# Kernel tuning notes

Measured on AMD Instinct MI355X. Metric: run time of the kernel, lower is better.

The kernel has to match this reference:

```python
import jax, jax.numpy as jnp
import numpy as np

K = 20
EPS = 1e-5
NEG_SLOPE = 0.2


def _graph_feature(x, k):
    # x: [B, N, C] -> edge features [B, N, k, 2C]
    xx = jnp.sum(x * x, axis=-1)                       # [B, N]
    inner = jnp.einsum('bnc,bmc->bnm', x, x)           # [B, N, N]
    neg_dist = 2.0 * inner - xx[:, :, None] - xx[:, None, :]
    idx = jax.lax.top_k(neg_dist, k)[1]                # [B, N, k] nearest neighbors
    nbr = jax.vmap(lambda f, i: f[i])(x, idx)          # [B, N, k, C]
    center = jnp.broadcast_to(x[:, :, None, :], nbr.shape)
    return jnp.concatenate([nbr - center, center], axis=-1)


def _bn(y, gamma, beta, axes):
    mu = y.mean(axes, keepdims=True)
    var = y.var(axes, keepdims=True)
    return (y - mu) * jax.lax.rsqrt(var + EPS) * gamma + beta


def _lrelu(y):
    return jnp.where(y > 0, y, NEG_SLOPE * y)


def _edge_block(feat, w, gamma, beta):
    # feat: [B, N, k, Cin], w: [Cout, Cin] (1x1 conv)
    y = jnp.einsum('bnkc,oc->bnko', feat, w)
    y = _lrelu(_bn(y, gamma, beta, (0, 1, 2)))
    return y.max(axis=2)                               # max over k -> [B, N, Cout]


def setup_inputs() -> dict:
    key = jax.random.key(0)
    ks = jax.random.split(key, 8)
    B, N = 16, 2048
    num_features = 128
    x = jax.random.normal(ks[0], (B, N, 3), dtype=jnp.float32)
    s = 0.05
    w1 = jax.random.normal(ks[1], (64, 6), dtype=jnp.float32) * s
    w2 = jax.random.normal(ks[2], (64, 128), dtype=jnp.float32) * s
    w3 = jax.random.normal(ks[3], (128, 128), dtype=jnp.float32) * s
    w4 = jax.random.normal(ks[4], (256, 256), dtype=jnp.float32) * s
    w5 = jax.random.normal(ks[5], (512, 512), dtype=jnp.float32) * s
    we = jax.random.normal(ks[6], (num_features, 512), dtype=jnp.float32) * s
    def gb(c):
        return jnp.ones((c,), jnp.float32), jnp.zeros((c,), jnp.float32)
    g1, b1 = gb(64); g2, b2 = gb(64); g3, b3 = gb(128); g4, b4 = gb(256); g5, b5 = gb(512)
    return dict(x=x, w1=w1, g1=g1, b1=b1, w2=w2, g2=g2, b2=b2, w3=w3, g3=g3, b3=b3,
                w4=w4, g4=g4, b4=b4, w5=w5, g5=g5, b5=b5, we=we)


def reference(x, w1, g1, b1, w2, g2, b2, w3, g3, b3, w4, g4, b4, w5, g5, b5, we):
    # x: [B, N, 3]
    x1 = _edge_block(_graph_feature(x, K), w1, g1, b1)    # [B, N, 64]
    x2 = _edge_block(_graph_feature(x1, K), w2, g2, b2)   # [B, N, 64]
    x3 = _edge_block(_graph_feature(x2, K), w3, g3, b3)   # [B, N, 128]
    x4 = _edge_block(_graph_feature(x3, K), w4, g4, b4)   # [B, N, 256]
    cat = jnp.concatenate([x1, x2, x3, x4], axis=-1)      # [B, N, 512]
    y = jnp.einsum('bnc,oc->bno', cat, w5)                # conv5 (1x1 conv1d)
    y = _lrelu(_bn(y, g5, b5, (0, 1)))
    y = y.max(axis=1)                                     # global max pool -> [B, 512]
    return y @ we.T                                       # embedding -> [B, num_features]
```

## Files before the change

kernel.cpp:

```cpp
#include <hip/hip_runtime.h>
#include <hip/hip_bf16.h>
#include <cstdint>

#define B_ 16
#define N_ 2048
#define KNN_K 20
#define EPS_ 1e-5f
#define SLOPE_ 0.2f
#define IMS 4.8828125e-4f

typedef __attribute__((ext_vector_type(4))) float f32x4;
typedef __attribute__((ext_vector_type(8))) short bf16x8;
typedef __attribute__((ext_vector_type(8))) _Float16 f16x8;

static __device__ __forceinline__ float lrelu(float v){ return v > 0.f ? v : SLOPE_*v; }

static __device__ __forceinline__ unsigned encf(float f){
  unsigned b = __float_as_uint(f);
  return (b & 0x80000000u) ? ~b : (b | 0x80000000u);
}
static __device__ __forceinline__ float decf(unsigned u){
  unsigned b = (u & 0x80000000u) ? (u ^ 0x80000000u) : ~u;
  return __uint_as_float(b);
}
static __device__ __forceinline__ short bfbits(float v){
  __hip_bfloat16 h = __float2bfloat16(v);
  return *reinterpret_cast<short*>(&h);
}
static __device__ __forceinline__ short h16(float v){
  _Float16 h = (_Float16)v;
  return *reinterpret_cast<short*>(&h);
}
static __device__ __forceinline__ float h2f(short s){
  _Float16 h = *reinterpret_cast<_Float16*>(&s);
  return (float)h;
}

template<int C, int CP>
__global__ __launch_bounds__(256) void convert_kernel(const float* __restrict__ f, int lda,
                                                      short* __restrict__ fbf, size_t plane,
                                                      float* __restrict__ xx){
  int wid  = (blockIdx.x * 256 + threadIdx.x) >> 6;
  int lane = threadIdx.x & 63;
  if (wid >= B_*N_) return;
  const float* p = f + (size_t)wid*lda;
  float s = 0.f;
  for (int c = lane; c < CP; c += 64){
    float v = (c < C) ? p[c] : 0.f;
    short h = h16(v);
    short m = h16((v - h2f(h)) * 2048.f);
    size_t o = (size_t)wid*CP + c;
    fbf[o] = h;
    fbf[plane + o] = m;
    s += v*v;
  }
  #pragma unroll
  for (int off=32; off; off>>=1) s += __shfl_down(s, off);
  if (lane==0) xx[wid] = s;
}

template<int CP>
__global__ __launch_bounds__(256) void knn_mfma(const short* __restrict__ fbf, size_t plane,
                                                const float* __restrict__ xx,
                                                float* __restrict__ pval, int* __restrict__ pidx){
  constexpr int SP = CP + 8;
  constexpr int CH = CP/8;
  constexpr int KC = CP/32;
  constexpr int PFH = CP/32;
  constexpr int FMBS = 2*64*SP;
  constexpr bool ALIAS = (FMBS*2 >= 64*65*4);
  constexpr unsigned LDSB = ALIAS ? (unsigned)(FMBS*2) : (unsigned)(FMBS*2 + 64*65*4);
  __shared__ __align__(16) char ldsbuf[LDSB];
  short* fmb = (short*)ldsbuf;
  float* dtile = ALIAS ? (float*)ldsbuf : (float*)(ldsbuf + FMBS*2);
  __shared__ float xm_s[64];

  int b   = blockIdx.x >> 6;
  int rem = blockIdx.x & 63;
  int n0  = (rem >> 1) << 6;
  int mh  = rem & 1;
  int mbase = mh << 10;
  int tid = threadIdx.x;
  int w    = tid >> 6;
  int lane = tid & 63;
  int fr = lane & 15, hi = lane >> 4;
  int r_loc = lane >> 2, csub = lane & 3;
  int gb = lane & 60;
  int myrow = w*16 + r_loc;
  size_t browoff = (size_t)b * N_;

  f16x8 aH[KC], aM[KC];
  {
    size_t arow = (browoff + n0 + w*16 + fr) * (size_t)CP;
    #pragma unroll
    for (int kc=0; kc<KC; ++kc){
      aH[kc] = *(const f16x8*)&fbf[arow + kc*32 + hi*8];
      aM[kc] = *(const f16x8*)&fbf[plane + arow + kc*32 + hi*8];
    }
  }

  float sv[5]; int si[5];
  #pragma unroll
  for (int j=0;j<5;++j){ sv[j] = -1e30f; si[j] = 0x7FFFFFFF; }

  int ldso[PFH];
  const short* gH[PFH];
  const short* gM[PFH];
  #pragma unroll
  for (int j=0;j<PFH;++j){
    int i = tid + j*256;
    int r = i/CH, cq = i - r*CH;
    ldso[j] = r*SP + cq*8;
    size_t g0 = (browoff + mbase + r)*(size_t)CP + cq*8;
    gH[j] = fbf + g0;
    gM[j] = fbf + plane + g0;
  }
  const float* xmp = xx + browoff + mbase + (tid & 63);
  float xmreg = 0.f;

  f16x8 pf[PFH];
  auto PFLOAD = [&](){
    #pragma unroll
    for (int j=0;j<PFH;++j) pf[j] = *(const f16x8*)gH[j];
    if (tid < 64) xmreg = *xmp;
  };
  auto WRITEPF = [&](){
    #pragma unroll
    for (int j=0;j<PFH;++j) *(f16x8*)&fmb[ldso[j]] = pf[j];
    #pragma unroll
    for (int j=0;j<PFH;++j){
      f16x8 v = *(const f16x8*)gM[j];
      *(f16x8*)&fmb[64*SP + ldso[j]] = v;
      gM[j] += 64*CP;
    }
    #pragma unroll
    for (int j=0;j<PFH;++j) gH[j] += 64*CP;
    if (tid < 64) xm_s[tid] = xmreg;
    xmp += 64;
  };

  PFLOAD();
  WRITEPF();
  __syncthreads();

  for (int mt = 0; mt < 16; ++mt){
    int m0 = mbase + (mt << 6);
    if (mt + 1 < 16) PFLOAD();

    f32x4 accH[4], accM[4];
    #pragma unroll
    for (int ct=0; ct<4; ++ct){ accH[ct] = (f32x4){0.f,0.f,0.f,0.f}; accM[ct] = accH[ct]; }
    const short* BH = fmb;
    const short* BM = fmb + 64*SP;
    #pragma unroll
    for (int kc = 0; kc < KC; ++kc){
      #pragma unroll
      for (int ct=0; ct<4; ++ct){
        int boff = (ct*16 + fr)*SP + kc*32 + hi*8;
        f16x8 bh = *(const f16x8*)&BH[boff];
        f16x8 bm = *(const f16x8*)&BM[boff];
        accH[ct] = __builtin_amdgcn_mfma_f32_16x16x32_f16(aH[kc], bh, accH[ct], 0,0,0);
        accM[ct] = __builtin_amdgcn_mfma_f32_16x16x32_f16(aM[kc], bh, accM[ct], 0,0,0);
        accM[ct] = __builtin_amdgcn_mfma_f32_16x16x32_f16(aH[kc], bm, accM[ct], 0,0,0);
      }
    }
    __syncthreads();

    #pragma unroll
    for (int reg=0; reg<4; ++reg){
      int nl = w*16 + hi*4 + reg;
      #pragma unroll
      for (int ct=0; ct<4; ++ct)
        dtile[nl*65 + ct*16 + fr] = 2.f*(accH[ct][reg] + IMS*accM[ct][reg]) - xm_s[ct*16 + fr];
    }

    int base = myrow*65 + csub*16;
    float thr = __shfl(sv[4], lane | 3);
    unsigned qm = 0u;
    #pragma unroll
    for (int jj=0; jj<16; ++jj){
      float v = dtile[base + jj];
      qm |= (v > thr) ? (1u << jj) : 0u;
    }
    unsigned long long bal = __ballot(qm != 0u);
    while (bal){
      unsigned nib = (unsigned)((bal >> gb) & 0xFull);
      int leader = nib ? (gb + (int)__builtin_ctz(nib)) : 64;
      int bbit = (int)__builtin_ctz(qm | 0x10000u);
      float mv = dtile[base + (bbit & 15)];
      int mid = m0 + (csub << 4) + bbit;
      float cv = __shfl(mv, leader);
      int   cid = __shfl(mid, leader);
      qm = (lane == leader) ? (qm & (qm - 1u)) : qm;
      int cnt = 0;
      #pragma unroll
      for (int j=0;j<5;++j) cnt += (sv[j] >= cv) ? 1 : 0;
      cnt += __shfl_xor(cnt, 1);
      cnt += __shfl_xor(cnt, 2);
      int pos = nib ? cnt : 20;
      float pv = __shfl_up(sv[4], 1);
      int   pi = __shfl_up(si[4], 1);
      #pragma unroll
      for (int j=0;j<5;++j){
        int g = csub*5 + j;
        float ns = (g < pos) ? sv[j] : ((g == pos) ? cv : pv);
        int   ni = (g < pos) ? si[j] : ((g == pos) ? cid : pi);
        pv = sv[j]; pi = si[j];
        sv[j] = ns; si[j] = ni;
      }
      bal = __ballot(qm != 0u);
    }

    if (mt + 1 < 16){
      if constexpr (ALIAS){
        __syncthreads();
        WRITEPF();
        __syncthreads();
      } else {
        WRITEPF();
        __syncthreads();
      }
    }
  }

  size_t orow = browoff + n0 + myrow;
  float* pvo = pval + (orow*2 + mh)*KNN_K + csub*5;
  int*   pio = pidx + (orow*2 + mh)*KNN_K + csub*5;
  #pragma unroll
  for (int j=0;j<5;++j){ pvo[j] = sv[j]; pio[j] = si[j]; }
}

__global__ __launch_bounds__(256) void knn_merge(const float* __restrict__ pval,
                                                 const int* __restrict__ pidx,
                                                 int* __restrict__ idxout){
  int r = blockIdx.x*256 + threadIdx.x;
  if (r >= B_*N_) return;
  const float* va = pval + (size_t)r*2*KNN_K;
  const float* vb = va + KNN_K;
  const int*   ia = pidx + (size_t)r*2*KNN_K;
  const int*   ib = ia + KNN_K;
  int i=0, j=0;
  #pragma unroll
  for (int t=0;t<KNN_K;++t){
    float a = va[i], bq = vb[j];
    bool ta = (a >= bq);
    idxout[(size_t)r*KNN_K + t] = ta ? ia[i] : ib[j];
    i += ta ? 1 : 0; j += ta ? 0 : 1;
  }
}

template<int CP>
__global__ __launch_bounds__(256) void gemm_pq(const short* __restrict__ fbf, size_t plane,
                                               const float* __restrict__ Wsrc, int wstride, int Cin,
                                               float* __restrict__ Out, int O){
  constexpr int BK = (CP < 64) ? CP : 64;
  constexpr int SP = BK + 8;
  __shared__ short Ah[128*SP];
  __shared__ short Am[128*SP];
  __shared__ short Wh[64*SP];
  __shared__ short Wm[64*SP];
  int obl = O >> 6;
  int bo = ((int)blockIdx.x % obl) << 6;
  int bm = ((int)blockIdx.x / obl) << 7;
  int tid = threadIdx.x;
  int w = tid >> 6, lane = tid & 63;
  int fr = lane & 15, hi = lane >> 4;
  f32x4 accH[2][4], accM[2][4];
  #pragma unroll
  for (int g=0; g<2; ++g)
    #pragma unroll
    for (int ct=0; ct<4; ++ct){ accH[g][ct] = (f32x4){0.f,0.f,0.f,0.f}; accM[g][ct] = accH[g][ct]; }

  for (int k0=0; k0<CP; k0+=BK){
    __syncthreads();
    for (int i=tid; i < 128*(BK/8); i += 256){
      int r = i/(BK/8), cq = i%(BK/8);
      size_t src = ((size_t)bm + r)*CP + k0 + cq*8;
      *(f16x8*)&Ah[r*SP + cq*8] = *(const f16x8*)&fbf[src];
      *(f16x8*)&Am[r*SP + cq*8] = *(const f16x8*)&fbf[plane + src];
    }
    for (int i=tid; i < 64*(BK/8); i += 256){
      int r = i/(BK/8), cq = i%(BK/8);
      f16x8 vh, vm;
      #pragma unroll
      for (int e=0;e<8;++e){
        int c = k0 + cq*8 + e;
        float v = (c < Cin) ? Wsrc[(size_t)(bo + r)*wstride + c] : 0.f;
        _Float16 h = (_Float16)v;
        vh[e] = h;
        vm[e] = (_Float16)((v - (float)h) * 2048.f);
      }
      *(f16x8*)&Wh[r*SP + cq*8] = vh;
      *(f16x8*)&Wm[r*SP + cq*8] = vm;
    }
    __syncthreads();
    #pragma unroll
    for (int kc=0; kc<BK/32; ++kc){
      f16x8 a0h = *(const f16x8*)&Ah[(w*32 +      fr)*SP + kc*32 + hi*8];
      f16x8 a0m = *(const f16x8*)&Am[(w*32 +      fr)*SP + kc*32 + hi*8];
      f16x8 a1h = *(const f16x8*)&Ah[(w*32 + 16 + fr)*SP + kc*32 + hi*8];
      f16x8 a1m = *(const f16x8*)&Am[(w*32 + 16 + fr)*SP + kc*32 + hi*8];
      #pragma unroll
      for (int ct=0; ct<4; ++ct){
        f16x8 bh = *(const f16x8*)&Wh[(ct*16 + fr)*SP + kc*32 + hi*8];
        f16x8 bm = *(const f16x8*)&Wm[(ct*16 + fr)*SP + kc*32 + hi*8];
        accH[0][ct] = __builtin_amdgcn_mfma_f32_16x16x32_f16(a0h, bh, accH[0][ct], 0,0,0);
        accM[0][ct] = __builtin_amdgcn_mfma_f32_16x16x32_f16(a0m, bh, accM[0][ct], 0,0,0);
        accM[0][ct] = __builtin_amdgcn_mfma_f32_16x16x32_f16(a0h, bm, accM[0][ct], 0,0,0);
        accH[1][ct] = __builtin_amdgcn_mfma_f32_16x16x32_f16(a1h, bh, accH[1][ct], 0,0,0);
        accM[1][ct] = __builtin_amdgcn_mfma_f32_16x16x32_f16(a1m, bh, accM[1][ct], 0,0,0);
        accM[1][ct] = __builtin_amdgcn_mfma_f32_16x16x32_f16(a1h, bm, accM[1][ct], 0,0,0);
      }
    }
  }
  #pragma unroll
  for (int g=0; g<2; ++g)
    #pragma unroll
    for (int ct=0; ct<4; ++ct)
      #pragma unroll
      for (int reg=0; reg<4; ++reg){
        int row = bm + w*32 + g*16 + hi*4 + reg;
        Out[(size_t)row*O + bo + ct*16 + fr] = accH[g][ct][reg] + IMS*accM[g][ct][reg];
      }
}

__global__ __launch_bounds__(256) void gemm_bf16(const float* __restrict__ A,
                                                 const float* __restrict__ Wt,
                                                 float* __restrict__ C){
  __shared__ short As[128*72];
  __shared__ short Bs[64*72];
  int bm = (int)(blockIdx.x >> 3) << 7;
  int bo = (int)(blockIdx.x & 7) << 6;
  int tid = threadIdx.x;
  int w = tid >> 6, lane = tid & 63;
  int fr = lane & 15, hi = lane >> 4;
  f32x4 acc[2][4];
  #pragma unroll
  for (int g=0; g<2; ++g)
    #pragma unroll
    for (int ct=0; ct<4; ++ct) acc[g][ct] = (f32x4){0.f,0.f,0.f,0.f};

  for (int k0=0; k0<512; k0+=64){
    __syncthreads();
    #pragma unroll 2
    for (int i = tid; i < 1024; i += 256){
      int r = i >> 3, cq = i & 7;
      const float* src = &A[(size_t)(bm + r)*512 + k0 + cq*8];
      bf16x8 v;
      #pragma unroll
      for (int e=0;e<8;++e) v[e] = bfbits(src[e]);
      *(bf16x8*)&As[r*72 + cq*8] = v;
    }
    #pragma unroll 2
    for (int i = tid; i < 512; i += 256){
      int r = i >> 3, cq = i & 7;
      const float* src = &Wt[(size_t)(bo + r)*512 + k0 + cq*8];
      bf16x8 v;
      #pragma unroll
      for (int e=0;e<8;++e) v[e] = bfbits(src[e]);
      *(bf16x8*)&Bs[r*72 + cq*8] = v;
    }
    __syncthreads();
    #pragma unroll
    for (int kc=0; kc<2; ++kc){
      bf16x8 a0 = *(const bf16x8*)&As[(w*32 +      fr)*72 + kc*32 + hi*8];
      bf16x8 a1 = *(const bf16x8*)&As[(w*32 + 16 + fr)*72 + kc*32 + hi*8];
      #pragma unroll
      for (int ct=0; ct<4; ++ct){
        bf16x8 bb = *(const bf16x8*)&Bs[(ct*16 + fr)*72 + kc*32 + hi*8];
        acc[0][ct] = __builtin_amdgcn_mfma_f32_16x16x32_bf16(a0, bb, acc[0][ct], 0,0,0);
        acc[1][ct] = __builtin_amdgcn_mfma_f32_16x16x32_bf16(a1, bb, acc[1][ct], 0,0,0);
      }
    }
  }
  #pragma unroll
  for (int g=0; g<2; ++g)
    #pragma unroll
    for (int ct=0; ct<4; ++ct)
      #pragma unroll
      for (int reg=0; reg<4; ++reg){
        int row = bm + w*32 + g*16 + hi*4 + reg;
        C[(size_t)row*512 + bo + ct*16 + fr] = acc[g][ct][reg];
      }
}

__global__ void wq_kernel(const float* __restrict__ w, float* __restrict__ wq, int Cin, int O){
  int i = blockIdx.x*blockDim.x + threadIdx.x;
  if (i >= O*Cin) return;
  int o = i / Cin, c = i - o*Cin;
  wq[i] = w[(size_t)o*2*Cin + Cin + c] - w[(size_t)o*2*Cin + c];
}

__global__ void zero_f_kernel(float* p, int n){
  int i = blockIdx.x*blockDim.x + threadIdx.x;
  if (i < n) p[i] = 0.f;
}
__global__ void zero_u_kernel(unsigned* p, int n){
  int i = blockIdx.x*blockDim.x + threadIdx.x;
  if (i < n) p[i] = 0u;
}

__global__ __launch_bounds__(256) void edge_agg(const float* __restrict__ P, const float* __restrict__ Q,
      const int* __restrict__ idx, const float* __restrict__ gamma,
      float* __restrict__ S, float* __restrict__ sums, float* __restrict__ sumsq, int O){
  const int ROWS = 64;
  int rpi = 256 / O;
  int iters = ROWS / rpi;
  int row0 = blockIdx.x * ROWS;
  int tid = threadIdx.x;
  int o  = tid % O;
  int rl = tid / O;
  int b  = row0 / N_;
  __shared__ int sidx[4][KNN_K];
  __shared__ float s1[256], s2[256];
  float g = gamma[o];
  float csum=0.f, csumsq=0.f;
  for (int it=0; it<iters; ++it){
    __syncthreads();
    if (tid < KNN_K*rpi) sidx[tid/KNN_K][tid%KNN_K] = idx[(size_t)(row0 + it*rpi)*KNN_K + tid];
    __syncthreads();
    int row = row0 + it*rpi + rl;
    float q = Q[(size_t)row*O + o];
    float mx=-1e30f, mn=1e30f, s=0.f, ss=0.f;
    #pragma unroll
    for (int k=0;k<KNN_K;++k){
      int m = sidx[rl][k];
      float p = P[((size_t)b*N_ + m)*O + o];
      mx = fmaxf(mx,p); mn = fminf(mn,p);
      float y = p + q; s += y; ss += y*y;
    }
    csum += s; csumsq += ss;
    S[(size_t)row*O + o] = (g >= 0.f ? mx : mn) + q;
  }
  s1[tid]=0.f; s2[tid]=0.f;
  __syncthreads();
  atomicAdd(&s1[o], csum); atomicAdd(&s2[o], csumsq);
  __syncthreads();
  if (tid < O){ atomicAdd(&sums[tid], s1[tid]); atomicAdd(&sumsq[tid], s2[tid]); }
}

__global__ void bn_finalize(const float* __restrict__ sums, const float* __restrict__ sumsq,
                            const float* __restrict__ gamma, const float* __restrict__ beta,
                            float invM, float* __restrict__ scale, float* __restrict__ shift, int O){
  int o = blockIdx.x*blockDim.x + threadIdx.x;
  if (o >= O) return;
  float mu = sums[o]*invM;
  float var = sumsq[o]*invM - mu*mu;
  float rs = rsqrtf(var + EPS_);
  float sc = gamma[o]*rs;
  scale[o] = sc; shift[o] = beta[o] - mu*sc;
}

__global__ void apply_write(const float* __restrict__ S, const float* __restrict__ scale,
                            const float* __restrict__ shift, float* __restrict__ cat, int off, int O){
  int i = blockIdx.x*blockDim.x + threadIdx.x;
  if (i >= B_*N_*O) return;
  int row = i / O, o = i - row*O;
  float v = S[i]*scale[o] + shift[o];
  cat[(size_t)row*512 + off + o] = lrelu(v);
}

__global__ __launch_bounds__(256) void conv5_stats(const float* __restrict__ Y, const float* __restrict__ g5,
      float* __restrict__ sums, float* __restrict__ sumsq, unsigned* __restrict__ maxenc){
  int bb = blockIdx.x / 16;
  int n0 = (blockIdx.x % 16) * 128;
  int tid = threadIdx.x;
  float s0=0.f, s1=0.f, q0=0.f, q1=0.f, m0=-1e30f, m1=-1e30f;
  float ga = g5[tid], gb = g5[tid+256];
  for (int n=0;n<128;++n){
    size_t base = ((size_t)bb*N_ + n0 + n)*512;
    float ya = Y[base + tid];
    float yb = Y[base + tid + 256];
    s0 += ya; q0 += ya*ya;
    s1 += yb; q1 += yb*yb;
    m0 = fmaxf(m0, ga>=0.f ? ya : -ya);
    m1 = fmaxf(m1, gb>=0.f ? yb : -yb);
  }
  atomicAdd(&sums[tid],      s0); atomicAdd(&sumsq[tid],      q0);
  atomicAdd(&sums[tid+256],  s1); atomicAdd(&sumsq[tid+256],  q1);
  atomicMax(&maxenc[bb*512 + tid],       encf(m0));
  atomicMax(&maxenc[bb*512 + tid + 256], encf(m1));
}

__global__ void pool_kernel(const unsigned* __restrict__ maxenc, const float* __restrict__ scale,
                            const float* __restrict__ shift, const float* __restrict__ g5,
                            float* __restrict__ pooled){
  int i = blockIdx.x*blockDim.x + threadIdx.x;
  if (i >= B_*512) return;
  int o = i & 511;
  float t = decf(maxenc[i]);
  float y = g5[o] >= 0.f ? t : -t;
  pooled[i] = lrelu(y*scale[o] + shift[o]);
}

__global__ void final_mm(const float* __restrict__ pooled, const float* __restrict__ we,
                         float* __restrict__ out){
  int i = blockIdx.x*blockDim.x + threadIdx.x;
  if (i >= B_*128) return;
  int b = i >> 7, j = i & 127;
  const float4* pp = (const float4*)(pooled + (size_t)b*512);
  const float4* wp = (const float4*)(we + (size_t)j*512);
  float s = 0.f;
  for (int c=0;c<128;++c){
    float4 a = pp[c], w = wp[c];
    s += a.x*w.x + a.y*w.y + a.z*w.z + a.w*w.w;
  }
  out[i] = s;
}

struct Ws {
  float* cat; float* P; float* Q; float* S; int* idx; float* xx;
  float* sums; float* sumsq; float* scale; float* shift;
  float* wq; unsigned* maxenc; float* pooled; short* fbf;
  float* pval; int* pidx;
};

template<int C, int CP>
static void run_layer(const Ws& W, const float* f, int lda, int O,
                      const float* w, const float* g, const float* bt,
                      int off_out, hipStream_t stream){
  const int M = B_*N_;
  size_t plane = (size_t)M*CP;
  convert_kernel<C, CP><<<M/4, 256, 0, stream>>>(f, lda, W.fbf, plane, W.xx);
  knn_mfma<CP><<<B_*(N_/64)*2, 256, 0, stream>>>(W.fbf, plane, W.xx, W.pval, W.pidx);
  knn_merge<<<(M+255)/256, 256, 0, stream>>>(W.pval, W.pidx, W.idx);
  int nwq = O*C;
  wq_kernel<<<(nwq+255)/256, 256, 0, stream>>>(w, W.wq, C, O);
  int grid = (M/128)*(O/64);
  gemm_pq<CP><<<grid, 256, 0, stream>>>(W.fbf, plane, w,    2*C, C, W.P, O);
  gemm_pq<CP><<<grid, 256, 0, stream>>>(W.fbf, plane, W.wq, C,   C, W.Q, O);
  zero_f_kernel<<<4, 256, 0, stream>>>(W.sums, 1024);
  edge_agg<<<M/64, 256, 0, stream>>>(W.P, W.Q, W.idx, g, W.S, W.sums, W.sumsq, O);
  bn_finalize<<<(O+255)/256, 256, 0, stream>>>(W.sums, W.sumsq, g, bt,
                                               1.f/((float)M*KNN_K), W.scale, W.shift, O);
  apply_write<<<(M*O+255)/256, 256, 0, stream>>>(W.S, W.scale, W.shift, W.cat, off_out, O);
}

extern "C" void kernel_launch(void* const* d_in, const int* in_sizes, int n_in,
                              void* d_out, int out_size, void* d_ws, size_t ws_size,
                              hipStream_t stream) {
  const float* x  = (const float*)d_in[0];
  const float* w1 = (const float*)d_in[1];
  const float* g1 = (const float*)d_in[2];
  const float* b1 = (const float*)d_in[3];
  const float* w2 = (const float*)d_in[4];
  const float* g2 = (const float*)d_in[5];
  const float* b2 = (const float*)d_in[6];
  const float* w3 = (const float*)d_in[7];
  const float* g3 = (const float*)d_in[8];
  const float* b3 = (const float*)d_in[9];
  const float* w4 = (const float*)d_in[10];
  const float* g4 = (const float*)d_in[11];
  const float* b4 = (const float*)d_in[12];
  const float* w5 = (const float*)d_in[13];
  const float* g5 = (const float*)d_in[14];
  const float* b5 = (const float*)d_in[15];
  const float* we = (const float*)d_in[16];

  char* ws = (char*)d_ws;
  Ws W;
  size_t off = 0;
  W.cat   = (float*)(ws + off); off += (size_t)16*2048*512*4;
  W.P     = (float*)(ws + off); off += (size_t)16*2048*256*4;
  W.Q     = (float*)(ws + off); off += (size_t)16*2048*256*4;
  W.S     = (float*)(ws + off); off += (size_t)16*2048*256*4;
  W.idx   = (int*)  (ws + off); off += (size_t)16*2048*20*4;
  W.xx    = (float*)(ws + off); off += (size_t)16*2048*4;
  W.sums  = (float*)(ws + off); off += 512*4;
  W.sumsq = (float*)(ws + off); off += 512*4;
  W.scale = (float*)(ws + off); off += 512*4;
  W.shift = (float*)(ws + off); off += 512*4;
  W.wq    = (float*)(ws + off); off += (size_t)256*128*4;
  W.maxenc= (unsigned*)(ws + off); off += (size_t)16*512*4;
  W.pooled= (float*)(ws + off); off += (size_t)16*512*4;
  W.fbf   = (short*)W.S;
  W.pval  = W.Q;
  W.pidx  = (int*)(W.Q + (size_t)2*16*2048*KNN_K);

  const int M = B_*N_;

  run_layer<3,   32>(W, x,           3,   64,  w1, g1, b1, 0,   stream);
  run_layer<64,  64>(W, W.cat,       512, 64,  w2, g2, b2, 64,  stream);
  run_layer<64,  64>(W, W.cat + 64,  512, 128, w3, g3, b3, 128, stream);
  run_layer<128,128>(W, W.cat + 128, 512, 256, w4, g4, b4, 256, stream);

  float* y5 = W.P;
  gemm_bf16<<<(M/128)*8, 256, 0, stream>>>(W.cat, w5, y5);
  zero_f_kernel<<<4, 256, 0, stream>>>(W.sums, 1024);
  zero_u_kernel<<<32, 256, 0, stream>>>(W.maxenc, 16*512);
  conv5_stats<<<B_*16, 256, 0, stream>>>(y5, g5, W.sums, W.sumsq, W.maxenc);
  bn_finalize<<<2, 256, 0, stream>>>(W.sums, W.sumsq, g5, b5, 1.f/(float)M, W.scale, W.shift, 512);
  pool_kernel<<<(16*512+255)/256, 256, 0, stream>>>(W.maxenc, W.scale, W.shift, g5, W.pooled);
  final_mm<<<(16*128+255)/256, 256, 0, stream>>>(W.pooled, we, (float*)d_out);
}
```

Baseline: 1.215 ms.

## Separate LDS buffers, prefetch both halves early, and rewrite top-k insertion as register max-selection

Gives the distance tile its own LDS region instead of aliasing the feature buffer, which removes one barrier per tile, and moves the low-part (M) global loads into the prefetch phase so both halves are issued before the MFMA loop. The threshold-ballot insertion loop is replaced by per-lane register candidates: each iteration picks the max over a row's four lanes, inserts it, and prunes candidates against the updated threshold. This adds register pressure and LDS usage, which may lower occupancy. The insertion loop may also run more iterations than before.

```diff
diff --git a/kernel.cpp b/kernel.cpp
--- a/kernel.cpp
+++ b/kernel.cpp
@@ -67,12 +67,8 @@
   constexpr int CH = CP/8;
   constexpr int KC = CP/32;
   constexpr int PFH = CP/32;
-  constexpr int FMBS = 2*64*SP;
-  constexpr bool ALIAS = (FMBS*2 >= 64*65*4);
-  constexpr unsigned LDSB = ALIAS ? (unsigned)(FMBS*2) : (unsigned)(FMBS*2 + 64*65*4);
-  __shared__ __align__(16) char ldsbuf[LDSB];
-  short* fmb = (short*)ldsbuf;
-  float* dtile = ALIAS ? (float*)ldsbuf : (float*)(ldsbuf + FMBS*2);
+  __shared__ __align__(16) short fmb[2*64*SP];
+  __shared__ float dtile[64*65];
   __shared__ float xm_s[64];
 
   int b   = blockIdx.x >> 6;
@@ -85,7 +81,6 @@
   int lane = tid & 63;
   int fr = lane & 15, hi = lane >> 4;
   int r_loc = lane >> 2, csub = lane & 3;
-  int gb = lane & 60;
   int myrow = w*16 + r_loc;
   size_t browoff = (size_t)b * N_;
 
@@ -105,36 +100,32 @@
 
   int ldso[PFH];
   const short* gH[PFH];
-  const short* gM[PFH];
   #pragma unroll
   for (int j=0;j<PFH;++j){
     int i = tid + j*256;
     int r = i/CH, cq = i - r*CH;
     ldso[j] = r*SP + cq*8;
-    size_t g0 = (browoff + mbase + r)*(size_t)CP + cq*8;
-    gH[j] = fbf + g0;
-    gM[j] = fbf + plane + g0;
+    gH[j] = fbf + (browoff + mbase + r)*(size_t)CP + cq*8;
   }
   const float* xmp = xx + browoff + mbase + (tid & 63);
   float xmreg = 0.f;
 
-  f16x8 pf[PFH];
+  f16x8 pf[PFH], pm[PFH];
   auto PFLOAD = [&](){
     #pragma unroll
-    for (int j=0;j<PFH;++j) pf[j] = *(const f16x8*)gH[j];
+    for (int j=0;j<PFH;++j){
+      pf[j] = *(const f16x8*)gH[j];
+      pm[j] = *(const f16x8*)(gH[j] + plane);
+    }
     if (tid < 64) xmreg = *xmp;
   };
   auto WRITEPF = [&](){
     #pragma unroll
-    for (int j=0;j<PFH;++j) *(f16x8*)&fmb[ldso[j]] = pf[j];
-    #pragma unroll
     for (int j=0;j<PFH;++j){
-      f16x8 v = *(const f16x8*)gM[j];
-      *(f16x8*)&fmb[64*SP + ldso[j]] = v;
-      gM[j] += 64*CP;
-    }
-    #pragma unroll
-    for (int j=0;j<PFH;++j) gH[j] += 64*CP;
+      *(f16x8*)&fmb[ldso[j]] = pf[j];
+      *(f16x8*)&fmb[64*SP + ldso[j]] = pm[j];
+      gH[j] += 64*CP;
+    }
     if (tid < 64) xm_s[tid] = xmreg;
     xmp += 64;
   };
@@ -164,8 +155,6 @@
         accM[ct] = __builtin_amdgcn_mfma_f32_16x16x32_f16(aH[kc], bm, accM[ct], 0,0,0);
       }
     }
-    __syncthreads();
-
     #pragma unroll
     for (int reg=0; reg<4; ++reg){
       int nl = w*16 + hi*4 + reg;
@@ -173,53 +162,57 @@
       for (int ct=0; ct<4; ++ct)
         dtile[nl*65 + ct*16 + fr] = 2.f*(accH[ct][reg] + IMS*accM[ct][reg]) - xm_s[ct*16 + fr];
     }
+    if (mt + 1 < 16) __syncthreads();
 
     int base = myrow*65 + csub*16;
-    float thr = __shfl(sv[4], lane | 3);
-    unsigned qm = 0u;
-    #pragma unroll
-    for (int jj=0; jj<16; ++jj){
-      float v = dtile[base + jj];
-      qm |= (v > thr) ? (1u << jj) : 0u;
-    }
-    unsigned long long bal = __ballot(qm != 0u);
-    while (bal){
-      unsigned nib = (unsigned)((bal >> gb) & 0xFull);
-      int leader = nib ? (gb + (int)__builtin_ctz(nib)) : 64;
-      int bbit = (int)__builtin_ctz(qm | 0x10000u);
-      float mv = dtile[base + (bbit & 15)];
-      int mid = m0 + (csub << 4) + bbit;
-      float cv = __shfl(mv, leader);
-      int   cid = __shfl(mid, leader);
-      qm = (lane == leader) ? (qm & (qm - 1u)) : qm;
+    float c[16];
+    #pragma unroll
+    for (int jj=0;jj<16;++jj) c[jj] = dtile[base + jj];
+    float t0 = fminf(sv[4], __shfl_xor(sv[4],1));
+    float thr = fminf(t0, __shfl_xor(t0,2));
+    #pragma unroll
+    for (int jj=0;jj<16;++jj) c[jj] = (c[jj] > thr) ? c[jj] : -3e38f;
+
+    while (true){
+      float lv = c[0]; int lj = 0;
+      #pragma unroll
+      for (int jj=1;jj<16;++jj){ bool bt = c[jj] > lv; lv = bt ? c[jj] : lv; lj = bt ? jj : lj; }
+      int lid = m0 + (csub<<4) + lj;
+      float rv = lv; int rid = lid;
+      { float ov = __shfl_xor(rv,1); int oid = __shfl_xor(rid,1);
+        bool tk = (ov > rv) || (ov == rv && oid < rid); rv = tk?ov:rv; rid = tk?oid:rid; }
+      { float ov = __shfl_xor(rv,2); int oid = __shfl_xor(rid,2);
+        bool tk = (ov > rv) || (ov == rv && oid < rid); rv = tk?ov:rv; rid = tk?oid:rid; }
+      if (!__ballot(rv > -2.9e38f)) break;
       int cnt = 0;
       #pragma unroll
-      for (int j=0;j<5;++j) cnt += (sv[j] >= cv) ? 1 : 0;
-      cnt += __shfl_xor(cnt, 1);
-      cnt += __shfl_xor(cnt, 2);
-      int pos = nib ? cnt : 20;
-      float pv = __shfl_up(sv[4], 1);
-      int   pi = __shfl_up(si[4], 1);
+      for (int j=0;j<5;++j) cnt += (sv[j] >= rv) ? 1 : 0;
+      cnt += __shfl_xor(cnt,1);
+      cnt += __shfl_xor(cnt,2);
+      int pos = (rv > -2.9e38f) ? cnt : 20;
+      float pvv = __shfl_up(sv[4],1);
+      int   pii = __shfl_up(si[4],1);
       #pragma unroll
       for (int j=0;j<5;++j){
         int g = csub*5 + j;
-        float ns = (g < pos) ? sv[j] : ((g == pos) ? cv : pv);
-        int   ni = (g < pos) ? si[j] : ((g == pos) ? cid : pi);
-        pv = sv[j]; pi = si[j];
+        float ns = (g < pos) ? sv[j] : ((g == pos) ? rv : pvv);
+        int   ni = (g < pos) ? si[j] : ((g == pos) ? rid : pii);
+        pvv = sv[j]; pii = si[j];
         sv[j] = ns; si[j] = ni;
       }
-      bal = __ballot(qm != 0u);
+      float u0 = fminf(sv[4], __shfl_xor(sv[4],1));
+      thr = fminf(u0, __shfl_xor(u0,2));
+      bool own = (lid == rid);
+      #pragma unroll
+      for (int jj=0;jj<16;++jj){
+        bool kill = (own && jj==lj) || !(c[jj] > thr);
+        c[jj] = kill ? -3e38f : c[jj];
+      }
     }
 
     if (mt + 1 < 16){
-      if constexpr (ALIAS){
-        __syncthreads();
-        WRITEPF();
-        __syncthreads();
-      } else {
-        WRITEPF();
-        __syncthreads();
-      }
+      WRITEPF();
+      __syncthreads();
     }
   }
 
```

New measurement: 1.861 ms. 1.53x slower.
